# Performance work log

Measured on AMD Instinct MI355X. Metric: run time of the kernel, lower is better.

Reference implementation:

```python
import jax, jax.numpy as jnp
import numpy as np
from jax import lax

SCALES = [0.5, 0.25, 0.125, 0.0625]
D_MODEL = 256
IN_CH = 1


def setup_inputs() -> dict:
    key = jax.random.key(0)
    ks = jax.random.split(key, 16)
    x = jax.random.normal(ks[0], (2, D_MODEL, 256, 256), dtype=jnp.float32)
    m = jax.random.uniform(ks[1], (2, IN_CH, 256, 256), dtype=jnp.float32)
    s = 0.05
    Wq = jax.random.normal(ks[2], (D_MODEL, D_MODEL, 1, 1), jnp.float32) * s
    bq = jax.random.normal(ks[3], (D_MODEL,), jnp.float32) * s
    Wk = jax.random.normal(ks[4], (D_MODEL, D_MODEL, 1, 1), jnp.float32) * s
    bk = jax.random.normal(ks[5], (D_MODEL,), jnp.float32) * s
    Wv = jax.random.normal(ks[6], (D_MODEL, D_MODEL, 1, 1), jnp.float32) * s
    bv = jax.random.normal(ks[7], (D_MODEL,), jnp.float32) * s
    Wmq = jax.random.normal(ks[8], (D_MODEL, IN_CH, 1, 1), jnp.float32) * s
    bmq = jax.random.normal(ks[9], (D_MODEL,), jnp.float32) * s
    Wmk = jax.random.normal(ks[10], (D_MODEL, IN_CH, 1, 1), jnp.float32) * s
    bmk = jax.random.normal(ks[11], (D_MODEL,), jnp.float32) * s
    Wo = jax.random.normal(ks[12], (D_MODEL, D_MODEL, 3, 3), jnp.float32) * s
    bo = jax.random.normal(ks[13], (D_MODEL,), jnp.float32) * s
    return {"x": x, "m": m, "Wq": Wq, "bq": bq, "Wk": Wk, "bk": bk,
            "Wv": Wv, "bv": bv, "Wmq": Wmq, "bmq": bmq, "Wmk": Wmk, "bmk": bmk,
            "Wo": Wo, "bo": bo, "b": 1, "c": 256}


def _conv1x1(z, W, bias):
    # W: (O, I, 1, 1)
    return jnp.einsum('bihw,oi->bohw', z, W[:, :, 0, 0]) + bias[None, :, None, None]


def _forward(x, m, Wq, bq, Wk, bk, Wv, bv, Wmq, bmq, Wmk, bmk, Wo, bo, b, c):
    bt, _, h, w = x.shape  # h, w are multiples of 64 -> pad is zero
    t = bt // b
    n_scales = len(SCALES)
    d_k = c // n_scales

    q = _conv1x1(x, Wq, bq)
    k = _conv1x1(x, Wk, bk)
    v = _conv1x1(x, Wv, bv)
    mq = _conv1x1(m, Wmq, bmq)
    mk = _conv1x1(m, Wmk, bmk)

    outs = []
    for i, scale in enumerate(SCALES):
        height, width = int(h * scale), int(w * scale)
        out_h, out_w = h // height, w // width
        sl = slice(i * d_k, (i + 1) * d_k)

        def patch(z):
            # (b, t, d_k, out_h, height, out_w, width) -> (b, t*out_h*out_w, d_k*height*width)
            z = z[:, sl].reshape(b, t, d_k, out_h, height, out_w, width)
            z = z.transpose(0, 1, 3, 5, 2, 4, 6)
            return z.reshape(b, t * out_h * out_w, d_k * height * width)

        Q, K, V = patch(q), patch(k), patch(v)
        MQ, MK = patch(mq), patch(mk)
        inv_sqrt_d = 1.0 / jnp.sqrt(jnp.asarray(Q.shape[-1], jnp.float32))
        scores = jnp.einsum('bnd,bmd->bnm', Q, K) * inv_sqrt_d
        mask_scores = jnp.einsum('bnd,bmd->bnm', MQ, MK) * inv_sqrt_d
        p_attn = jax.nn.softmax(scores * mask_scores, axis=-1)
        y = jnp.einsum('bnm,bmd->bnd', p_attn, V)
        # back to (bt, d_k, h, w)
        y = y.reshape(b, t, out_h, out_w, d_k, height, width)
        y = y.transpose(0, 1, 4, 2, 5, 3, 6).reshape(bt, d_k, h, w)
        outs.append(y)

    out = jnp.concatenate(outs, axis=1)
    z = lax.conv_general_dilated(out, Wo, window_strides=(1, 1),
                                 padding=((1, 1), (1, 1)),
                                 dimension_numbers=('NCHW', 'OIHW', 'NCHW'))
    z = z + bo[None, :, None, None]
    return jnp.where(z > 0, z, 0.2 * z)  # LeakyReLU(0.2)


def reference(x, m, Wq, bq, Wk, bk, Wv, bv, Wmq, bmq, Wmk, bmk, Wo, bo, b, c):
    return _forward(x, m, Wq, bq, Wk, bk, Wv, bv, Wmq, bmq, Wmk, bmk, Wo, bo, b, c)
```

## Files before the change

### kernel.cpp

```cpp
#include <hip/hip_runtime.h>
#include <stdint.h>


typedef __attribute__((ext_vector_type(8))) short short8;
typedef __attribute__((ext_vector_type(4))) float floatx4;
typedef __attribute__((ext_vector_type(4))) unsigned int uintx4;

#define DEV static __device__ __forceinline__

DEV unsigned short f2bf(float f) {
  unsigned u = __builtin_bit_cast(unsigned, f);
  unsigned r = u + 0x7FFFu + ((u >> 16) & 1u);
  return (unsigned short)(r >> 16);
}

DEV void patch_row(int n, int sc, int lw, int& pt, int& sp0) {
  pt = n >> (2 + 2 * sc);
  int rem = n & ((4 << (2 * sc)) - 1);
  int oh = rem >> (1 + sc), ow = rem & ((2 << sc) - 1);
  sp0 = (oh << (lw + 8)) + (ow << lw);
}

__global__ void k_prep_w(const float* __restrict__ Wq, const float* __restrict__ Wk,
                         const float* __restrict__ Wv, const float* __restrict__ bq,
                         const float* __restrict__ bk, const float* __restrict__ bv,
                         const float* __restrict__ Wmq, const float* __restrict__ bmq,
                         const float* __restrict__ Wmk, const float* __restrict__ bmk,
                         unsigned short* __restrict__ wqkv, float* __restrict__ bias,
                         float* __restrict__ msc) {
  int b = blockIdx.x;
  int t = threadIdx.x;
  if (b < 768) {
    const float* src = b < 256 ? (Wq + b * 256) : (b < 512 ? (Wk + (b - 256) * 256)
                                                           : (Wv + (b - 512) * 256));
    wqkv[b * 256 + t] = f2bf(src[t]);
    if (t == 0) bias[b] = b < 256 ? bq[b] : (b < 512 ? bk[b - 256] : bv[b - 512]);
  } else {
    int sc = t >> 6, lane = t & 63;
    int ch = sc * 64 + lane;
    float a0 = Wmq[ch] * Wmk[ch];
    float a1 = Wmq[ch] * bmk[ch];
    float a2 = bmq[ch] * Wmk[ch];
    float a3 = bmq[ch] * bmk[ch];
    for (int off = 32; off; off >>= 1) {
      a0 += __shfl_xor(a0, off); a1 += __shfl_xor(a1, off);
      a2 += __shfl_xor(a2, off); a3 += __shfl_xor(a3, off);
    }
    if (lane == 0) {
      msc[sc * 4 + 0] = a0; msc[sc * 4 + 1] = a1;
      msc[sc * 4 + 2] = a2; msc[sc * 4 + 3] = a3;
    }
  }
}

__global__ void k_prep_wo(const float* __restrict__ Wo, unsigned short* __restrict__ wobf,
                          float* __restrict__ scoresG, unsigned int* __restrict__ pbuf) {
  int blk = blockIdx.x;
  if (blk < 2304) {
    int didx = blk >> 8, o = blk & 255, c = threadIdx.x;
    wobf[didx * 65536 + o * 256 + c] = f2bf(Wo[o * 2304 + c * 9 + didx]);
  } else {
    int i = (blk - 2304) * 256 + threadIdx.x;
    if (i < 559232) scoresG[i] = 0.f;
    if (i < 140032) pbuf[i] = 0u;
  }
}

__global__ __launch_bounds__(256) void k_xt(const float* __restrict__ x,
                                            unsigned short* __restrict__ xt) {
  __shared__ __align__(16) unsigned short tile[64][72];
  int p0 = blockIdx.x * 64, c0 = blockIdx.y * 64, t = blockIdx.z;
  int tid = threadIdx.x;
  {
    int cc = tid >> 2, pq = (tid & 3) * 16;
    const float* src = x + ((t * 256 + c0 + cc) * 65536 + p0 + pq);
    __align__(16) unsigned short tmp[16];
#pragma unroll
    for (int e = 0; e < 16; e += 4) {
      floatx4 v = *(const floatx4*)(src + e);
      tmp[e + 0] = f2bf(v[0]); tmp[e + 1] = f2bf(v[1]);
      tmp[e + 2] = f2bf(v[2]); tmp[e + 3] = f2bf(v[3]);
    }
    *(uintx4*)&tile[cc][pq] = *(const uintx4*)&tmp[0];
    *(uintx4*)&tile[cc][pq + 8] = *(const uintx4*)&tmp[8];
  }
  __syncthreads();
  {
    int pp = tid >> 2, cg = (tid & 3) * 16;
    __align__(16) unsigned short outv[16];
#pragma unroll
    for (int e = 0; e < 16; ++e) outv[e] = tile[cg + e][pp];
    unsigned short* dst = xt + ((t * 65536 + p0 + pp) * 256 + c0 + cg);
    *(uintx4*)dst = *(const uintx4*)&outv[0];
    *(uintx4*)(dst + 8) = *(const uintx4*)&outv[8];
  }
}

__global__ __launch_bounds__(256) void k_yt(const unsigned short* __restrict__ ynat,
                                            unsigned short* __restrict__ yt) {
  __shared__ __align__(16) unsigned short tile[64][72];
  int p0 = blockIdx.x * 64, c0 = blockIdx.y * 64, t = blockIdx.z;
  int tid = threadIdx.x;
  {
    int cc = tid >> 2, pq = (tid & 3) * 16;
    const unsigned short* src = ynat + ((t * 256 + c0 + cc) * 65536 + p0 + pq);
    *(uintx4*)&tile[cc][pq] = *(const uintx4*)src;
    *(uintx4*)&tile[cc][pq + 8] = *(const uintx4*)(src + 8);
  }
  __syncthreads();
  {
    int pp = tid >> 2, cg = (tid & 3) * 16;
    __align__(16) unsigned short outv[16];
#pragma unroll
    for (int e = 0; e < 16; ++e) outv[e] = tile[cg + e][pp];
    unsigned short* dst = yt + ((t * 65536 + p0 + pp) * 256 + c0 + cg);
    *(uintx4*)dst = *(const uintx4*)&outv[0];
    *(uintx4*)(dst + 8) = *(const uintx4*)&outv[8];
  }
}

__global__ __launch_bounds__(256) void k_qkv(const unsigned short* __restrict__ xt,
                                             const unsigned short* __restrict__ wqkv,
                                             const float* __restrict__ bias,
                                             unsigned short* __restrict__ qkv) {
  __shared__ __align__(16) unsigned short As[128][64];
  __shared__ __align__(16) unsigned short Bs[128][64];
  int flat = blockIdx.x + (blockIdx.y << 10);
  int lg = ((flat & 7) * 768) + (flat >> 3);
  int n_t = lg / 6, m_t = lg - n_t * 6;
  int n0 = n_t << 7, m0 = m_t << 7;
  int tid = threadIdx.x;
  int w = tid >> 6, l = tid & 63;
  int wr = w >> 1, wc = w & 1;
  int l15 = l & 15, lhi = l >> 4;
  int sr = tid >> 1, sbase = (tid & 1) * 4, r7 = sr & 7;
  const unsigned short* gA = wqkv + (m0 + sr) * 256 + sbase * 8;
  const unsigned short* gB = xt + (n0 + sr) * 256 + sbase * 8;
  floatx4 zf = {0.f, 0.f, 0.f, 0.f};
  floatx4 acc[4][4];
#pragma unroll
  for (int i = 0; i < 4; ++i)
#pragma unroll
    for (int j = 0; j < 4; ++j) acc[i][j] = zf;
  uintx4 ra[4], rb[4];
#define QLOAD(K0) { const uintx4* pa = (const uintx4*)(gA + (K0)); \
                    const uintx4* pb = (const uintx4*)(gB + (K0)); \
                    ra[0] = pa[0]; ra[1] = pa[1]; ra[2] = pa[2]; ra[3] = pa[3]; \
                    rb[0] = pb[0]; rb[1] = pb[1]; rb[2] = pb[2]; rb[3] = pb[3]; }
  QLOAD(0);
#pragma unroll
  for (int ch = 0; ch < 4; ++ch) {
    __syncthreads();
#pragma unroll
    for (int j = 0; j < 4; ++j) {
      *(uintx4*)&As[sr][((sbase + j) ^ r7) * 8] = ra[j];
      *(uintx4*)&Bs[sr][((sbase + j) ^ r7) * 8] = rb[j];
    }
    __syncthreads();
    if (ch < 3) QLOAD((ch + 1) * 64);
#pragma unroll
    for (int kk = 0; kk < 2; ++kk) {
      short8 af[4], bfr[4];
#pragma unroll
      for (int f = 0; f < 4; ++f) {
        int arow = wr * 64 + f * 16 + l15;
        af[f] = *(const short8*)&As[arow][(((kk << 2) + lhi) ^ (arow & 7)) * 8];
        int brow = wc * 64 + f * 16 + l15;
        bfr[f] = *(const short8*)&Bs[brow][(((kk << 2) + lhi) ^ (brow & 7)) * 8];
      }
#pragma unroll
      for (int fm = 0; fm < 4; ++fm)
#pragma unroll
        for (int fn = 0; fn < 4; ++fn)
          acc[fm][fn] = __builtin_amdgcn_mfma_f32_16x16x32_bf16(af[fm], bfr[fn], acc[fm][fn], 0, 0, 0);
    }
  }
#undef QLOAD
#pragma unroll
  for (int fm = 0; fm < 4; ++fm) {
    int crow = m0 + wr * 64 + fm * 16 + lhi * 4;
#pragma unroll
    for (int rr = 0; rr < 4; ++rr) {
      float bv = bias[crow + rr];
#pragma unroll
      for (int fn = 0; fn < 4; ++fn) {
        int pcol = n0 + wc * 64 + fn * 16 + l15;
        int t = pcol >> 16, p = pcol & 65535;
        qkv[(t * 768 + crow + rr) * 65536 + p] = f2bf(acc[fm][fn][rr] + bv);
      }
    }
  }
}

__global__ __launch_bounds__(256) void k_gram2(const float* __restrict__ m,
                                               float* __restrict__ G) {
  __shared__ __align__(16) float Ns[32][68];
  __shared__ __align__(16) float Ms[32][68];
  int bid = blockIdx.x;
  int sc, tn, tm, z, nchunks, soff;
  if (bid < 32)      { sc = 0; tn = 0; tm = 0; z = bid;      nchunks = 8; soff = 0; }
  else if (bid < 40) { sc = 1; tn = 0; tm = 0; z = bid - 32; nchunks = 8; soff = 64; }
  else if (bid < 72) { int r = bid - 40; int tl = r >> 1; sc = 2; tn = tl >> 2; tm = tl & 3; z = r & 1; nchunks = 8; soff = 1088; }
  else               { int tl = bid - 72; sc = 3; tn = tl >> 4; tm = tl & 15; z = 0; nchunks = 4; soff = 17472; }
  int lw = 7 - sc, W = 1 << lw, N = 8 << (2 * sc);
  int kbase = z * nchunks * 64;
  int n0 = tn * 32, m0 = tm * 32;
  int tid = threadIdx.x;
  bool isA = tid < 128;
  int u = tid & 127;
  int srow = u >> 2, sslot0 = (u & 3) * 4;
  int grow = (isA ? n0 : m0) + srow;
  bool valid = grow < N;
  int pt = 0, sp0 = 0;
  if (valid) patch_row(grow, sc, lw, pt, sp0);
  int gbase = pt * 65536 + sp0;
  int trc = tid >> 4, tcc = tid & 15;
  float a00 = 0.f, a01 = 0.f, a10 = 0.f, a11 = 0.f;
  floatx4 zf = {0.f, 0.f, 0.f, 0.f};
  for (int c = 0; c < nchunks; ++c) {
    int k0 = kbase + c * 64;
    floatx4 v[4];
#pragma unroll
    for (int j = 0; j < 4; ++j) {
      v[j] = zf;
      if (valid) {
        int s = k0 + (sslot0 + j) * 4;
        int hh = s >> lw, ww = s & (W - 1);
        v[j] = *(const floatx4*)(m + gbase + (hh << 8) + ww);
      }
    }
    __syncthreads();
    float* dstrow = isA ? &Ns[srow][0] : &Ms[srow][0];
#pragma unroll
    for (int j = 0; j < 4; ++j) *(floatx4*)&dstrow[(sslot0 + j) * 4] = v[j];
    __syncthreads();
#pragma unroll 4
    for (int k = 0; k < 64; k += 4) {
      floatx4 na = *(const floatx4*)&Ns[2 * trc][k];
      floatx4 nb = *(const floatx4*)&Ns[2 * trc + 1][k];
      floatx4 ma = *(const floatx4*)&Ms[2 * tcc][k];
      floatx4 mb = *(const floatx4*)&Ms[2 * tcc + 1][k];
#pragma unroll
      for (int e = 0; e < 4; ++e) {
        a00 += na[e] * ma[e]; a01 += na[e] * mb[e];
        a10 += nb[e] * ma[e]; a11 += nb[e] * mb[e];
      }
    }
  }
  int rn = n0 + 2 * trc, rm = m0 + 2 * tcc;
  float res[2][2] = {{a00, a01}, {a10, a11}};
#pragma unroll
  for (int i = 0; i < 2; ++i)
#pragma unroll
    for (int j = 0; j < 2; ++j) {
      if (rn + i < N && rm + j < N) {
        float* dst = &G[soff + (rn + i) * N + rm + j];
        if (sc < 3) atomicAdd(dst, res[i][j]); else *dst = res[i][j];
      }
    }
}

__global__ void k_rsum(const float* __restrict__ m, float* __restrict__ rbuf) {
  int row = blockIdx.x, lane = threadIdx.x;
  int sc, n;
  if (row < 8)        { sc = 0; n = row; }
  else if (row < 40)  { sc = 1; n = row - 8; }
  else if (row < 168) { sc = 2; n = row - 40; }
  else                { sc = 3; n = row - 168; }
  int lw = 7 - sc, W = 1 << lw;
  int pt, sp0;
  patch_row(n, sc, lw, pt, sp0);
  int base = pt * 65536 + sp0;
  int S = 1 << (14 - 2 * sc);
  float acc = 0.f;
  for (int s = lane; s < S; s += 64) {
    int hh = s >> lw, ww = s & (W - 1);
    acc += m[base + (hh << 8) + ww];
  }
  for (int off = 32; off; off >>= 1) acc += __shfl_xor(acc, off);
  if (lane == 0) rbuf[row] = acc;
}

__global__ __launch_bounds__(256) void k_scores2(const unsigned short* __restrict__ qkv,
                                                 float* __restrict__ scores) {
  __shared__ __align__(16) unsigned short As[32][136];
  __shared__ __align__(16) unsigned short Bs[32][136];
  int bid = blockIdx.x;
  int sc, tn, tm, z, soff;
  if (bid < 256)      { sc = 0; tn = 0; tm = 0; z = bid;       soff = 0; }
  else if (bid < 320) { sc = 1; tn = 0; tm = 0; z = bid - 256; soff = 64; }
  else if (bid < 576) { int r = bid - 320; int tl = r >> 4; sc = 2; tn = tl >> 2; tm = tl & 3; z = r & 15; soff = 1088; }
  else                { int r = bid - 576; int tl = r >> 2; sc = 3; tn = tl >> 4; tm = tl & 15; z = r & 3; soff = 17472; }
  int lw = 7 - sc, W = 1 << lw, lS = 14 - 2 * sc, N = 8 << (2 * sc);
  int n0 = tn * 32, m0 = tm * 32;
  int kbase = z * 4096;
  int tid = threadIdx.x, w = tid >> 6, l = tid & 63;
  int wr = w >> 1, wc = w & 1, l15 = l & 15, lhi = l >> 4;
  floatx4 acc = {0.f, 0.f, 0.f, 0.f};
  bool isA = tid < 128;
  int u = tid & 127;
  int srow = u >> 2, sslot0 = (u & 3) * 4;
  int grow = (isA ? n0 : m0) + srow;
  int cb = (isA ? 0 : 256) + sc * 64;
  int pt = 0, sp0 = 0;
  bool valid = grow < N;
  if (valid) patch_row(grow, sc, lw, pt, sp0);
  int rowbase = (pt * 768 + cb) * 65536 + sp0;
  uintx4 zu = {0u, 0u, 0u, 0u};
  uintx4 r[4];
#define SLOAD(KS) { int kb2 = kbase + (KS) * 128; \
  _Pragma("unroll") for (int j = 0; j < 4; ++j) { \
    uintx4 v = zu; \
    if (valid) { int k = kb2 + (sslot0 + j) * 8; \
      int cl = k >> lS; int s = k & ((1 << lS) - 1); \
      int hh = s >> lw, ww = s & (W - 1); \
      v = *(const uintx4*)(qkv + rowbase + cl * 65536 + (hh << 8) + ww); } \
    r[j] = v; } }
  SLOAD(0);
  for (int ks = 0; ks < 32; ++ks) {
    __syncthreads();
    {
      unsigned short* dstrow = isA ? &As[srow][0] : &Bs[srow][0];
#pragma unroll
      for (int j = 0; j < 4; ++j) *(uintx4*)&dstrow[(sslot0 + j) * 8] = r[j];
    }
    __syncthreads();
    if (ks < 31) SLOAD(ks + 1);
#pragma unroll
    for (int kk = 0; kk < 4; ++kk) {
      short8 a = *(const short8*)&As[wr * 16 + l15][(kk * 4 + lhi) * 8];
      short8 b = *(const short8*)&Bs[wc * 16 + l15][(kk * 4 + lhi) * 8];
      acc = __builtin_amdgcn_mfma_f32_16x16x32_bf16(a, b, acc, 0, 0, 0);
    }
  }
#undef SLOAD
  int rrow = n0 + wr * 16 + lhi * 4;
  int ccol = m0 + wc * 16 + l15;
  if (ccol < N) {
#pragma unroll
    for (int rr = 0; rr < 4; ++rr)
      if (rrow + rr < N) atomicAdd(&scores[soff + (rrow + rr) * N + ccol], acc[rr]);
  }
}

__global__ void k_softmax(const float* __restrict__ scores, const float* __restrict__ G,
                          const float* __restrict__ rbuf, const float* __restrict__ msc,
                          unsigned short* __restrict__ pbuf) {
  int row = blockIdx.x, lane = threadIdx.x;
  int sc, n, roff, soff, poff;
  if (row < 8)        { sc = 0; n = row;       roff = 0;   soff = 0;     poff = 0; }
  else if (row < 40)  { sc = 1; n = row - 8;   roff = 8;   soff = 64;    poff = 512; }
  else if (row < 168) { sc = 2; n = row - 40;  roff = 40;  soff = 1088;  poff = 1536; }
  else                { sc = 3; n = row - 168; roff = 168; soff = 17472; poff = 17920; }
  int N = 8 << (2 * sc);
  int Kpad = (sc < 2) ? 32 : N;
  float Sf = (float)(1 << (14 - 2 * sc));
  float invD = 1.0f / (float)(1 << (20 - 2 * sc));
  float alpha = msc[sc * 4 + 0], beta = msc[sc * 4 + 1];
  float gamma = msc[sc * 4 + 2], delta = msc[sc * 4 + 3];
  float rn = rbuf[roff + n];
  float vals[8];
  float mx = -1e30f;
#pragma unroll
  for (int j = 0; j < 8; ++j) {
    float v = -1e30f;
    int mcol = lane + j * 64;
    if (j * 64 < N && mcol < N) {
      float sq = scores[soff + n * N + mcol];
      float g = G[soff + n * N + mcol];
      float rm = rbuf[roff + mcol];
      v = sq * (alpha * g + beta * rn + gamma * rm + delta * Sf) * invD;
    }
    vals[j] = v;
    mx = fmaxf(mx, v);
  }
  for (int off = 32; off; off >>= 1) mx = fmaxf(mx, __shfl_xor(mx, off));
  float sum = 0.f;
#pragma unroll
  for (int j = 0; j < 8; ++j) {
    int mcol = lane + j * 64;
    float e = 0.f;
    if (j * 64 < N && mcol < N) e = __expf(vals[j] - mx);
    vals[j] = e;
    sum += e;
  }
  for (int off = 32; off; off >>= 1) sum += __shfl_xor(sum, off);
  float inv = 1.f / sum;
#pragma unroll
  for (int j = 0; j < 8; ++j) {
    int mcol = lane + j * 64;
    if (j * 64 < N && mcol < N) pbuf[poff + n * Kpad + mcol] = f2bf(vals[j] * inv);
  }
}

__global__ __launch_bounds__(256) void k_pv(const unsigned short* __restrict__ qkv,
                                            const unsigned short* __restrict__ pbuf,
                                            unsigned short* __restrict__ ynat) {
  int bid = blockIdx.x;
  int sc, bx, by;
  if (bid < 4096)      { sc = 0; bx = bid; by = 0; }
  else if (bid < 6144) { sc = 1; bx = bid - 4096; by = 0; }
  else if (bid < 8192) { int r = bid - 6144; sc = 2; bx = r >> 1; by = r & 1; }
  else                 { int r = bid - 8192; sc = 3; bx = r >> 3; by = r & 7; }
  int WR    = (sc == 0) ? 1 : (sc == 1) ? 2 : 4;
  int logWC = (sc == 0) ? 2 : (sc == 1) ? 1 : 0;
  int poff  = (sc == 0) ? 0 : (sc == 1) ? 512 : (sc == 2) ? 1536 : 17920;
  int lw = 7 - sc, W = 1 << lw;
  int lS = 14 - 2 * sc;
  int N = 8 << (2 * sc);
  int Kpad = (sc < 2) ? 32 : N;
  int WC = 1 << logWC;
  int d0 = bx * (WC * 64);
  int nb = by * (WR * 16);
  __shared__ __align__(16) unsigned short As[64][40];
  __shared__ __align__(16) unsigned short Bt[256][32];
  int tid = threadIdx.x;
  int w = tid >> 6, l = tid & 63;
  int wr = w >> logWC, wc = w & (WC - 1);
  int l15 = l & 15, lhi = l >> 4;
  floatx4 zf = {0.f, 0.f, 0.f, 0.f};
  floatx4 acc[4];
#pragma unroll
  for (int i = 0; i < 4; ++i) acc[i] = zf;
  int bmp = tid & 15;
  int dg = tid >> 4;
  bool act0 = (WC > 1) || (dg < 8);
  bool has1 = (WC == 4);
  bool doA = tid < WR * 64;
  int arow = tid >> 2, akg = (tid & 3) * 8;
  int ksteps = Kpad >> 5;
  uintx4 zu = {0u, 0u, 0u, 0u};
  int vcb = (512 + sc * 64) * 65536;

  for (int ks = 0; ks < ksteps; ++ks) {
    int k0 = ks * 32;
    uintx4 av = zu;
    if (doA) av = *(const uintx4*)(pbuf + poff + (nb + arow) * Kpad + k0 + akg);
    int gm0 = k0 + 2 * bmp, gm1 = gm0 + 1;
    bool mv0 = gm0 < N, mv1 = gm1 < N;
    int pt0 = 0, sp00 = 0, pt1 = 0, sp01 = 0;
    if (mv0) patch_row(gm0, sc, lw, pt0, sp00);
    if (mv1) patch_row(gm1, sc, lw, pt1, sp01);
    uintx4 lo0 = zu, hi0 = zu, lo1 = zu, hi1 = zu;
    {
      int d = d0 + dg * 8;
      int cl = d >> lS;
      int s = d & ((1 << lS) - 1);
      int hh = s >> lw, ww = s & (W - 1);
      int sp = (hh << 8) + ww;
      if (act0 && mv0) lo0 = *(const uintx4*)(qkv + pt0 * 768 * 65536 + vcb + cl * 65536 + sp00 + sp);
      if (act0 && mv1) hi0 = *(const uintx4*)(qkv + pt1 * 768 * 65536 + vcb + cl * 65536 + sp01 + sp);
    }
    if (has1) {
      int d = d0 + (dg + 16) * 8;
      int cl = d >> lS;
      int s = d & ((1 << lS) - 1);
      int hh = s >> lw, ww = s & (W - 1);
      int sp = (hh << 8) + ww;
      if (mv0) lo1 = *(const uintx4*)(qkv + pt0 * 768 * 65536 + vcb + cl * 65536 + sp00 + sp);
      if (mv1) hi1 = *(const uintx4*)(qkv + pt1 * 768 * 65536 + vcb + cl * 65536 + sp01 + sp);
    }
    __syncthreads();
    if (doA) *(uintx4*)&As[arow][akg] = av;
    if (act0) {
      int du = dg * 8;
#pragma unroll
      for (int j = 0; j < 8; ++j) {
        int d = du + j;
        unsigned losh = (lo0[j >> 1] >> ((j & 1) * 16)) & 0xFFFFu;
        unsigned hish = (hi0[j >> 1] >> ((j & 1) * 16)) & 0xFFFFu;
        unsigned wv = losh | (hish << 16);
        int slot = (bmp >> 2) ^ ((d >> 1) & 3) ^ ((d >> 3) & 3);
        ((unsigned int*)&Bt[d][0])[slot * 4 + (bmp & 3)] = wv;
      }
    }
    if (has1) {
      int du = (dg + 16) * 8;
#pragma unroll
      for (int j = 0; j < 8; ++j) {
        int d = du + j;
        unsigned losh = (lo1[j >> 1] >> ((j & 1) * 16)) & 0xFFFFu;
        unsigned hish = (hi1[j >> 1] >> ((j & 1) * 16)) & 0xFFFFu;
        unsigned wv = losh | (hish << 16);
        int slot = (bmp >> 2) ^ ((d >> 1) & 3) ^ ((d >> 3) & 3);
        ((unsigned int*)&Bt[d][0])[slot * 4 + (bmp & 3)] = wv;
      }
    }
    __syncthreads();
    short8 a = *(const short8*)&As[wr * 16 + l15][lhi * 8];
#pragma unroll
    for (int fn = 0; fn < 4; ++fn) {
      int row = wc * 64 + fn * 16 + l15;
      int slot = lhi ^ ((row >> 1) & 3) ^ ((row >> 3) & 3);
      short8 b = *(const short8*)&Bt[row][slot * 8];
      acc[fn] = __builtin_amdgcn_mfma_f32_16x16x32_bf16(a, b, acc[fn], 0, 0, 0);
    }
    __syncthreads();
  }
  int nrow = nb + wr * 16 + lhi * 4;
#pragma unroll
  for (int rr = 0; rr < 4; ++rr) {
    int n = nrow + rr;
    if (n < N) {
      int pt, sp0;
      patch_row(n, sc, lw, pt, sp0);
#pragma unroll
      for (int fn = 0; fn < 4; ++fn) {
        int d = d0 + wc * 64 + fn * 16 + l15;
        int cl = d >> lS;
        int s = d & ((1 << lS) - 1);
        int hh = s >> lw, ww = s & (W - 1);
        int c = sc * 64 + cl;
        ynat[(pt * 256 + c) * 65536 + sp0 + (hh << 8) + ww] = f2bf(acc[fn][rr]);
      }
    }
  }
}

__global__ __launch_bounds__(256, 2) void k_conv(const unsigned short* __restrict__ yt,
                                                 const unsigned short* __restrict__ wo,
                                                 const float* __restrict__ bo,
                                                 float* __restrict__ out) {
  __shared__ __align__(16) unsigned short As[128][64];
  __shared__ __align__(16) unsigned short Bs[256][64];
  int flat = blockIdx.x;
  int lg = ((flat & 7) << 7) + (flat >> 3);
  int n_t = lg >> 1, m_t = lg & 1;
  int n0 = n_t << 8, m0 = m_t << 7;
  int tt = n0 >> 16, yy = (n0 >> 8) & 255;
  int tid = threadIdx.x;
  int w = tid >> 6, l = tid & 63;
  int wr = w >> 1, wc = w & 1;
  int l15 = l & 15, lhi = l >> 4;
  int arow = tid >> 1, ahalf = tid & 1;
  floatx4 zf = {0.f, 0.f, 0.f, 0.f};
  floatx4 acc[4][8];
#pragma unroll
  for (int i = 0; i < 4; ++i)
#pragma unroll
    for (int j = 0; j < 8; ++j) acc[i][j] = zf;
  uintx4 zu = {0u, 0u, 0u, 0u};
  uintx4 rb[8];
#define CLOADB(LC) { int didx = (LC) >> 2; int cc = ((LC) & 3) << 6; \
    int dy3 = (didx * 11) >> 5; int dy = dy3 - 1; int dx = didx - dy3 * 3 - 1; \
    int yq = yy + dy, xq = tid + dx; \
    if (((unsigned)yq < 256u) && ((unsigned)xq < 256u)) { \
      const uintx4* pb = (const uintx4*)(yt + ((((tt << 8) + yq) << 8) + xq) * 256 + cc); \
      rb[0] = pb[0]; rb[1] = pb[1]; rb[2] = pb[2]; rb[3] = pb[3]; \
      rb[4] = pb[4]; rb[5] = pb[5]; rb[6] = pb[6]; rb[7] = pb[7]; \
    } else { rb[0] = zu; rb[1] = zu; rb[2] = zu; rb[3] = zu; \
             rb[4] = zu; rb[5] = zu; rb[6] = zu; rb[7] = zu; } }
  CLOADB(0);
  for (int s = 0; s < 36; ++s) {
    __syncthreads();
    {
      int r7 = tid & 7;
#pragma unroll
      for (int j = 0; j < 8; ++j)
        *(uintx4*)&Bs[tid][(j ^ r7) * 8] = rb[j];
      int didx = s >> 2, cc = (s & 3) << 6;
      const uintx4* pa = (const uintx4*)(wo + didx * 65536 + (m0 + arow) * 256 + cc + ahalf * 32);
      uintx4 ra0 = pa[0], ra1 = pa[1], ra2 = pa[2], ra3 = pa[3];
      int a7 = arow & 7;
      *(uintx4*)&As[arow][((ahalf * 4 + 0) ^ a7) * 8] = ra0;
      *(uintx4*)&As[arow][((ahalf * 4 + 1) ^ a7) * 8] = ra1;
      *(uintx4*)&As[arow][((ahalf * 4 + 2) ^ a7) * 8] = ra2;
      *(uintx4*)&As[arow][((ahalf * 4 + 3) ^ a7) * 8] = ra3;
    }
    __syncthreads();
    if (s < 35) CLOADB(s + 1);
#pragma unroll
    for (int kk = 0; kk < 2; ++kk) {
      short8 af[4];
#pragma unroll
      for (int f = 0; f < 4; ++f) {
        int ar = wr * 64 + f * 16 + l15;
        af[f] = *(const short8*)&As[ar][(((kk << 2) + lhi) ^ (ar & 7)) * 8];
      }
#pragma unroll
      for (int fn = 0; fn < 8; ++fn) {
        int br = wc * 128 + fn * 16 + l15;
        short8 b = *(const short8*)&Bs[br][(((kk << 2) + lhi) ^ (br & 7)) * 8];
#pragma unroll
        for (int fm = 0; fm < 4; ++fm)
          acc[fm][fn] = __builtin_amdgcn_mfma_f32_16x16x32_bf16(af[fm], b, acc[fm][fn], 0, 0, 0);
      }
    }
  }
#undef CLOADB
#pragma unroll
  for (int fm = 0; fm < 4; ++fm) {
    int o = m0 + wr * 64 + fm * 16 + lhi * 4;
#pragma unroll
    for (int rr = 0; rr < 4; ++rr) {
      float bias = bo[o + rr];
#pragma unroll
      for (int fn = 0; fn < 8; ++fn) {
        int xcol = wc * 128 + fn * 16 + l15;
        float z = acc[fm][fn][rr] + bias;
        out[((tt * 256 + o + rr) << 16) + (yy << 8) + xcol] = z > 0.f ? z : 0.2f * z;
      }
    }
  }
}

extern "C" void kernel_launch(void* const* d_in, const int* in_sizes, int n_in,
                              void* d_out, int out_size, void* d_ws, size_t ws_size,
                              hipStream_t stream) {
  const float* x   = (const float*)d_in[0];
  const float* m   = (const float*)d_in[1];
  const float* Wq  = (const float*)d_in[2];
  const float* bq  = (const float*)d_in[3];
  const float* Wk  = (const float*)d_in[4];
  const float* bk  = (const float*)d_in[5];
  const float* Wv  = (const float*)d_in[6];
  const float* bv  = (const float*)d_in[7];
  const float* Wmq = (const float*)d_in[8];
  const float* bmq = (const float*)d_in[9];
  const float* Wmk = (const float*)d_in[10];
  const float* bmk = (const float*)d_in[11];
  const float* Wo  = (const float*)d_in[12];
  const float* bo  = (const float*)d_in[13];

  char* ws = (char*)d_ws;
  unsigned short* qkv   = (unsigned short*)(ws);
  unsigned short* xt    = (unsigned short*)(ws + 201326592);
  unsigned short* wqkv  = (unsigned short*)(ws + 268435456);
  unsigned short* wobf  = (unsigned short*)(ws + 268828672);
  float* bias           = (float*)(ws + 270008320);
  float* msc            = (float*)(ws + 270011392);
  float* scores         = (float*)(ws + 270011456);
  float* G              = (float*)(ws + 271129920);
  float* rbuf           = (float*)(ws + 272248384);
  unsigned short* pbuf  = (unsigned short*)(ws + 272251104);
  float* out            = (float*)d_out;
  unsigned short* ynat  = (unsigned short*)d_out;
  unsigned short* yt    = xt;

  k_prep_w<<<dim3(769), dim3(256), 0, stream>>>(Wq, Wk, Wv, bq, bk, bv, Wmq, bmq, Wmk, bmk,
                                                wqkv, bias, msc);
  k_prep_wo<<<dim3(4489), dim3(256), 0, stream>>>(Wo, wobf, scores, (unsigned int*)pbuf);
  k_xt<<<dim3(1024, 4, 2), dim3(256), 0, stream>>>(x, xt);
  k_qkv<<<dim3(1024, 6), dim3(256), 0, stream>>>(xt, wqkv, bias, qkv);
  k_gram2<<<dim3(328), dim3(256), 0, stream>>>(m, G);
  k_rsum<<<dim3(680), dim3(64), 0, stream>>>(m, rbuf);
  k_scores2<<<dim3(1600), dim3(256), 0, stream>>>(qkv, scores);
  k_softmax<<<dim3(680), dim3(64), 0, stream>>>(scores, G, rbuf, msc, pbuf);
  k_pv<<<dim3(10240), dim3(256), 0, stream>>>(qkv, pbuf, ynat);
  k_yt<<<dim3(1024, 4, 2), dim3(256), 0, stream>>>(ynat, yt);
  k_conv<<<dim3(1024), dim3(256), 0, stream>>>(yt, wobf, bo, out);
}
```

Measured before the change: 616.3 us.

## Reuse one input row tile across the three horizontal conv taps

The 3x3 output conv kernel now loads one halo-extended row of the bf16 activations (258 pixels x 32 channels) per stage. It reuses that row for all three dx taps by shifting the B-fragment read in shared memory, instead of reloading a separate 256x64 tile for each tap. The A tile now holds the weights for all three dx taps of a given dy. This cuts global reads of the activation tensor by about three times, and the loop drops from 36 to 24 stages. In exchange the indexing is more complex, the halo load is split across extra threads, and the odd shifted rows may hit shared-memory bank conflicts.

```diff
diff --git a/kernel.cpp b/kernel.cpp
--- a/kernel.cpp
+++ b/kernel.cpp
@@ -521,8 +521,8 @@
                                                  const unsigned short* __restrict__ wo,
                                                  const float* __restrict__ bo,
                                                  float* __restrict__ out) {
-  __shared__ __align__(16) unsigned short As[128][64];
-  __shared__ __align__(16) unsigned short Bs[256][64];
+  __shared__ __align__(16) unsigned short As[128][128];
+  __shared__ __align__(16) unsigned short Bs[130][64];
   int flat = blockIdx.x;
   int lg = ((flat & 7) << 7) + (flat >> 3);
   int n_t = lg >> 1, m_t = lg & 1;
@@ -532,7 +532,9 @@
   int w = tid >> 6, l = tid & 63;
   int wr = w >> 1, wc = w & 1;
   int l15 = l & 15, lhi = l >> 4;
-  int arow = tid >> 1, ahalf = tid & 1;
+  int a_d0 = tid >> 7, a_o0 = tid & 127;
+  bool doA1 = tid < 128;
+  bool doBh = tid >= 254;
   floatx4 zf = {0.f, 0.f, 0.f, 0.f};
   floatx4 acc[4][8];
 #pragma unroll
@@ -540,54 +542,74 @@
 #pragma unroll
     for (int j = 0; j < 8; ++j) acc[i][j] = zf;
   uintx4 zu = {0u, 0u, 0u, 0u};
-  uintx4 rb[8];
-#define CLOADB(LC) { int didx = (LC) >> 2; int cc = ((LC) & 3) << 6; \
-    int dy3 = (didx * 11) >> 5; int dy = dy3 - 1; int dx = didx - dy3 * 3 - 1; \
-    int yq = yy + dy, xq = tid + dx; \
-    if (((unsigned)yq < 256u) && ((unsigned)xq < 256u)) { \
-      const uintx4* pb = (const uintx4*)(yt + ((((tt << 8) + yq) << 8) + xq) * 256 + cc); \
-      rb[0] = pb[0]; rb[1] = pb[1]; rb[2] = pb[2]; rb[3] = pb[3]; \
-      rb[4] = pb[4]; rb[5] = pb[5]; rb[6] = pb[6]; rb[7] = pb[7]; \
-    } else { rb[0] = zu; rb[1] = zu; rb[2] = zu; rb[3] = zu; \
-             rb[4] = zu; rb[5] = zu; rb[6] = zu; rb[7] = zu; } }
-  CLOADB(0);
-  for (int s = 0; s < 36; ++s) {
+  uintx4 rb[4], ra0[4], ra1[4];
+  const unsigned short* ybase = yt + (tt << 24);
+#define CLOAD(ST) { \
+    int dy = (ST) >> 3, cc = ((ST) & 7) << 5; \
+    int yq = yy + dy - 1; \
+    bool yv = (unsigned)yq < 256u; \
+    { int xq = tid - 1; \
+      if (yv && (unsigned)xq < 256u) { \
+        const uintx4* p = (const uintx4*)(ybase + ((yq << 8) + xq) * 256 + cc); \
+        rb[0] = p[0]; rb[1] = p[1]; rb[2] = p[2]; rb[3] = p[3]; \
+      } else { rb[0] = zu; rb[1] = zu; rb[2] = zu; rb[3] = zu; } } \
+    { const uintx4* p = (const uintx4*)(wo + (dy * 3 + a_d0) * 65536 + (m0 + a_o0) * 256 + cc); \
+      ra0[0] = p[0]; ra0[1] = p[1]; ra0[2] = p[2]; ra0[3] = p[3]; } \
+    if (doA1) { \
+      const uintx4* p = (const uintx4*)(wo + (dy * 3 + 2) * 65536 + (m0 + tid) * 256 + cc); \
+      ra1[0] = p[0]; ra1[1] = p[1]; ra1[2] = p[2]; ra1[3] = p[3]; \
+    } else if (doBh) { \
+      int xq = tid + 1;   \
+      if (yv && xq < 256) { \
+        const uintx4* p = (const uintx4*)(ybase + ((yq << 8) + xq) * 256 + cc); \
+        ra1[0] = p[0]; ra1[1] = p[1]; ra1[2] = p[2]; ra1[3] = p[3]; \
+      } else { ra1[0] = zu; ra1[1] = zu; ra1[2] = zu; ra1[3] = zu; } } }
+  CLOAD(0);
+  for (int st = 0; st < 24; ++st) {
     __syncthreads();
     {
-      int r7 = tid & 7;
-#pragma unroll
-      for (int j = 0; j < 8; ++j)
-        *(uintx4*)&Bs[tid][(j ^ r7) * 8] = rb[j];
-      int didx = s >> 2, cc = (s & 3) << 6;
-      const uintx4* pa = (const uintx4*)(wo + didx * 65536 + (m0 + arow) * 256 + cc + ahalf * 32);
-      uintx4 ra0 = pa[0], ra1 = pa[1], ra2 = pa[2], ra3 = pa[3];
-      int a7 = arow & 7;
-      *(uintx4*)&As[arow][((ahalf * 4 + 0) ^ a7) * 8] = ra0;
-      *(uintx4*)&As[arow][((ahalf * 4 + 1) ^ a7) * 8] = ra1;
-      *(uintx4*)&As[arow][((ahalf * 4 + 2) ^ a7) * 8] = ra2;
-      *(uintx4*)&As[arow][((ahalf * 4 + 3) ^ a7) * 8] = ra3;
-    }
-    __syncthreads();
-    if (s < 35) CLOADB(s + 1);
-#pragma unroll
-    for (int kk = 0; kk < 2; ++kk) {
+      int brow = tid >> 1, bhf = (tid & 1) * 4, br7 = brow & 7;
+#pragma unroll
+      for (int j = 0; j < 4; ++j)
+        *(uintx4*)&Bs[brow][((bhf + j) ^ br7) * 8] = rb[j];
+      int ao7 = a_o0 & 7;
+#pragma unroll
+      for (int j = 0; j < 4; ++j)
+        *(uintx4*)&As[a_o0][((a_d0 * 4 + j) ^ ao7) * 8] = ra0[j];
+      if (doA1) {
+        int o7 = tid & 7;
+#pragma unroll
+        for (int j = 0; j < 4; ++j)
+          *(uintx4*)&As[tid][((8 + j) ^ o7) * 8] = ra1[j];
+      } else if (doBh) {
+        int xh = tid + 2;
+        int brow2 = xh >> 1, bhf2 = (xh & 1) * 4, br72 = brow2 & 7;
+#pragma unroll
+        for (int j = 0; j < 4; ++j)
+          *(uintx4*)&Bs[brow2][((bhf2 + j) ^ br72) * 8] = ra1[j];
+      }
+    }
+    __syncthreads();
+    if (st < 23) CLOAD(st + 1);
+#pragma unroll
+    for (int dx = 0; dx < 3; ++dx) {
       short8 af[4];
 #pragma unroll
       for (int f = 0; f < 4; ++f) {
-        int ar = wr * 64 + f * 16 + l15;
-        af[f] = *(const short8*)&As[ar][(((kk << 2) + lhi) ^ (ar & 7)) * 8];
+        int ol = wr * 64 + f * 16 + l15;
+        af[f] = *(const short8*)&As[ol][((dx * 4 + lhi) ^ (ol & 7)) * 8];
       }
 #pragma unroll
       for (int fn = 0; fn < 8; ++fn) {
-        int br = wc * 128 + fn * 16 + l15;
-        short8 b = *(const short8*)&Bs[br][(((kk << 2) + lhi) ^ (br & 7)) * 8];
+        int xh = wc * 128 + fn * 16 + l15 + dx;
+        short8 b = *(const short8*)&Bs[xh >> 1][((((xh & 1) * 4 + lhi)) ^ ((xh >> 1) & 7)) * 8];
 #pragma unroll
         for (int fm = 0; fm < 4; ++fm)
           acc[fm][fn] = __builtin_amdgcn_mfma_f32_16x16x32_bf16(af[fm], b, acc[fm][fn], 0, 0, 0);
       }
     }
   }
-#undef CLOADB
+#undef CLOAD
 #pragma unroll
   for (int fm = 0; fm < 4; ++fm) {
     int o = m0 + wr * 64 + fm * 16 + lhi * 4;
```

Result: faster. 568.4 us (-7.8%).
